# Performance work log

Measured on AMD Instinct MI355X. Metric: run time of the kernel, lower is better.

Reference implementation:

```python
import jax, jax.numpy as jnp
import numpy as np

K = 512
DIM = 256
BETA = 0.25


def setup_inputs() -> dict:
    key = jax.random.key(0)
    k1, k2 = jax.random.split(key)
    x = jax.random.normal(k1, (64, DIM, 32, 32), dtype=jnp.float32)
    lookup_table = jax.random.normal(k2, (K, DIM), dtype=jnp.float32)
    return {"x": x, "lookup_table": lookup_table}


def reference(x, lookup_table):
    b, d, h, w = x.shape
    # [b,d,h,w] -> [b*h*w, d]
    xf = jnp.transpose(x, (0, 2, 3, 1)).reshape(-1, d)
    # Squared Euclidean distances (argmin identical to torch.cdist argmin)
    d2 = (
        jnp.sum(xf * xf, axis=-1, keepdims=True)
        - 2.0 * (xf @ lookup_table.T)
        + jnp.sum(lookup_table * lookup_table, axis=-1)
    )  # [N, K]
    q = jnp.argmin(d2, axis=1)  # [N]
    x_e = lookup_table[q].reshape(b, h, w, d).transpose(0, 3, 1, 2)  # [b,d,h,w]
    q_x = q.reshape(b, h, w)
    codebook_loss = jnp.mean(jnp.square(jax.lax.stop_gradient(x) - x_e))
    commitment_loss = jnp.mean(jnp.square(x - jax.lax.stop_gradient(x_e)))
    loss = codebook_loss + BETA * commitment_loss
    return x_e, q_x, loss
```

## Files before the change

### kernel.cpp

```cpp
#include <hip/hip_runtime.h>

#define DIM     256
#define HW      1024
#define N_ROWS  65536
#define NT      256
#define QBM     64
#define NBLK    1024
#define MARGIN  0.0625f

#define OUT_Q_OFF    16777216
#define OUT_LOSS_OFF 16842752

#define WS_DIST   512
#define WS_X2     1536
#define WS_CNT_I  3072
#define WS_LIST_I 4096
#define WS_LUTBF_B 524288

#define VQ_LDS 73728

typedef __attribute__((ext_vector_type(8))) short short8v;
typedef __attribute__((ext_vector_type(4))) float floatx4;

#define GLOAD_LDS16(gaddr, laddr) \
    __builtin_amdgcn_global_load_lds((const __attribute__((address_space(1))) unsigned int*)(gaddr), \
                                     (__attribute__((address_space(3))) unsigned int*)(laddr), 16, 0, 0)

__device__ __forceinline__ unsigned short bf16_rne(float f) {
    unsigned int u = __float_as_uint(f);
    u += 0x7fffu + ((u >> 16) & 1u);
    return (unsigned short)(u >> 16);
}
__device__ __forceinline__ float bf16_to_f(unsigned short h) {
    return __uint_as_float(((unsigned int)h) << 16);
}
__device__ __forceinline__ uint4 pack8(const unsigned short* h) {
    uint4 u;
    u.x = (unsigned)h[0] | ((unsigned)h[1] << 16);
    u.y = (unsigned)h[2] | ((unsigned)h[3] << 16);
    u.z = (unsigned)h[4] | ((unsigned)h[5] << 16);
    u.w = (unsigned)h[6] | ((unsigned)h[7] << 16);
    return u;
}

__global__ void c2_kernel(const float* __restrict__ lut, float* __restrict__ ws) {
    if (threadIdx.x == 0) ((int*)ws)[WS_CNT_I] = 0;
    int t = threadIdx.x;
    for (int k = t; k < 512; k += 256) {
        const float4* row = (const float4*)(lut + (size_t)k * DIM);
        float s = 0.f;
        #pragma unroll 8
        for (int i = 0; i < DIM / 4; ++i) {
            float4 v = row[i];
            s += v.x * v.x + v.y * v.y + v.z * v.z + v.w * v.w;
        }
        ws[k] = s;
    }
}

__global__ void lutprep_kernel(const float* __restrict__ lut, float* __restrict__ ws) {
    int g = blockIdx.x * 256 + threadIdx.x;
    int lane = g & 63;
    int ctu  = (g >> 6) & 31;
    int dcg  = g >> 11;
    int code = ctu * 16 + (lane & 15);
    int d0   = dcg * 32 + (lane >> 4) * 8;
    const float* src = lut + (size_t)code * DIM + d0;
    unsigned short hi[8], lo[8];
    #pragma unroll
    for (int j = 0; j < 8; ++j) {
        float v = src[j];
        unsigned short h = bf16_rne(v);
        hi[j] = h;
        lo[j] = bf16_rne(v - bf16_to_f(h));
    }
    char* dst = (char*)ws + WS_LUTBF_B + (size_t)((dcg * 32 + ctu) * 2) * 1024 + lane * 16;
    *(uint4*)dst          = pack8(hi);
    *(uint4*)(dst + 1024) = pack8(lo);
}

__global__ __launch_bounds__(NT, 2) void vq_kernel(const float* __restrict__ x,
                                                   const float* __restrict__ lut,
                                                   float* __restrict__ out,
                                                   float* __restrict__ ws) {
    extern __shared__ char smem[];

    const char* lutbf = (const char*)ws + WS_LUTBF_B;

    const int tid = threadIdx.x;
    const int blk = blockIdx.x;
    const int n0  = blk * QBM;
    const int b   = n0 >> 10;
    const int hw0 = n0 & 1023;
    const float* xb = x + (size_t)b * (DIM * HW) + hw0;

    const int wave = tid >> 6;
    const int lane = tid & 63;
    const int l15  = lane & 15;
    const int l4   = lane >> 4;
    const int cg   = wave;

    const int srt  = tid >> 6;
    char* awr_hi = smem + 65536 + srt * 2048 + lane * 16;
    const int arow = srt * 16 + l15;
    const int ad0  = l4 * 8;

    float x2local = 0.f;
    floatx4 acc[4][8];
    #pragma unroll
    for (int i = 0; i < 4; ++i)
        #pragma unroll
        for (int j = 0; j < 8; ++j) acc[i][j] = (floatx4)0.f;

    {
        #pragma unroll
        for (int i = 0; i < 16; ++i) {
            int cc = (tid >> 6) * 16 + i;
            GLOAD_LDS16(lutbf + (size_t)(0 * 64 + cc) * 1024 + lane * 16, smem + cc * 1024);
        }
        const float* src = xb + (size_t)ad0 * HW + arow;
        unsigned short hi[8], lo[8];
        #pragma unroll
        for (int e = 0; e < 8; ++e) {
            float v = src[(size_t)e * HW];
            x2local = fmaf(v, v, x2local);
            unsigned short h = bf16_rne(v);
            hi[e] = h;
            lo[e] = bf16_rne(v - bf16_to_f(h));
        }
        *(uint4*)awr_hi          = pack8(hi);
        *(uint4*)(awr_hi + 1024) = pack8(lo);
    }
    __syncthreads();

    for (int dc = 0; dc < 8; ++dc) {
        short8v ah[4], al[4];
        #pragma unroll
        for (int rtl = 0; rtl < 4; ++rtl) {
            const char* ra = smem + 65536 + rtl * 2048 + lane * 16;
            ah[rtl] = *(const short8v*)ra;
            al[rtl] = *(const short8v*)(ra + 1024);
        }
        short8v bh[8], bl[8];
        #pragma unroll
        for (int ct = 0; ct < 8; ++ct) {
            const char* bp = smem + (size_t)((cg * 8 + ct) * 2) * 1024 + lane * 16;
            bh[ct] = *(const short8v*)bp;
            bl[ct] = *(const short8v*)(bp + 1024);
        }
        __builtin_amdgcn_sched_barrier(0);
        asm volatile("s_waitcnt lgkmcnt(0)" ::: "memory");
        __builtin_amdgcn_sched_barrier(0);
        __builtin_amdgcn_s_barrier();
        __builtin_amdgcn_sched_barrier(0);
        float xn[8];
        if (dc < 7) {
            #pragma unroll
            for (int i = 0; i < 16; ++i) {
                int cc = (tid >> 6) * 16 + i;
                GLOAD_LDS16(lutbf + (size_t)((dc + 1) * 64 + cc) * 1024 + lane * 16, smem + cc * 1024);
            }
            const float* src = xb + (size_t)((dc + 1) * 32 + ad0) * HW + arow;
            #pragma unroll
            for (int e = 0; e < 8; ++e) xn[e] = src[(size_t)e * HW];
        }
        __builtin_amdgcn_s_setprio(1);
        #pragma unroll
        for (int ct = 0; ct < 8; ++ct)
            #pragma unroll
            for (int rtl = 0; rtl < 4; ++rtl)
                acc[rtl][ct] = __builtin_amdgcn_mfma_f32_16x16x32_bf16(ah[rtl], bh[ct], acc[rtl][ct], 0, 0, 0);
        #pragma unroll
        for (int ct = 0; ct < 8; ++ct)
            #pragma unroll
            for (int rtl = 0; rtl < 4; ++rtl)
                acc[rtl][ct] = __builtin_amdgcn_mfma_f32_16x16x32_bf16(al[rtl], bh[ct], acc[rtl][ct], 0, 0, 0);
        #pragma unroll
        for (int ct = 0; ct < 8; ++ct)
            #pragma unroll
            for (int rtl = 0; rtl < 4; ++rtl)
                acc[rtl][ct] = __builtin_amdgcn_mfma_f32_16x16x32_bf16(ah[rtl], bl[ct], acc[rtl][ct], 0, 0, 0);
        __builtin_amdgcn_s_setprio(0);
        if (dc < 7) {
            unsigned short hi[8], lo[8];
            #pragma unroll
            for (int e = 0; e < 8; ++e) {
                float v = xn[e];
                x2local = fmaf(v, v, x2local);
                unsigned short h = bf16_rne(v);
                hi[e] = h;
                lo[e] = bf16_rne(v - bf16_to_f(h));
            }
            *(uint4*)awr_hi          = pack8(hi);
            *(uint4*)(awr_hi + 1024) = pack8(lo);
        }
        __syncthreads();
    }

    float* redv1 = (float*)smem;
    float* redv2 = (float*)(smem + 1024);
    int*   redi1 = (int*)(smem + 2048);
    int*   qsh   = (int*)(smem + 3072);
    float* wsumx = (float*)(smem + 3328);

    #pragma unroll
    for (int rtl = 0; rtl < 4; ++rtl) {
        #pragma unroll
        for (int r = 0; r < 4; ++r) {
            float v1 = 3.4e38f, v2 = 3.4e38f; int i1 = 0;
            #pragma unroll
            for (int ct = 0; ct < 8; ++ct) {
                int code = (cg * 8 + ct) * 16 + l15;
                float dist = fmaf(-2.f, acc[rtl][ct][r], ws[code]);
                if (dist < v1) { v2 = v1; v1 = dist; i1 = code; }
                else if (dist < v2) v2 = dist;
            }
            #pragma unroll
            for (int off = 1; off < 16; off <<= 1) {
                float ov1 = __shfl_xor(v1, off, 64);
                int   oi1 = __shfl_xor(i1, off, 64);
                float ov2 = __shfl_xor(v2, off, 64);
                float nv2 = fminf(fmaxf(v1, ov1), fminf(v2, ov2));
                if (ov1 < v1 || (ov1 == v1 && oi1 < i1)) { v1 = ov1; i1 = oi1; }
                v2 = nv2;
            }
            if (l15 == 0) {
                int idx = cg * 64 + rtl * 16 + l4 * 4 + r;
                redv1[idx] = v1; redi1[idx] = i1; redv2[idx] = v2;
            }
        }
    }
    __syncthreads();

    float dist_part = 0.f;
    if (tid < QBM) {
        const int row = tid;
        float v1 = redv1[row]; int i1 = redi1[row]; float v2 = redv2[row];
        #pragma unroll
        for (int s = 1; s < 4; ++s) {
            float ov1 = redv1[s * 64 + row]; int oi1 = redi1[s * 64 + row]; float ov2 = redv2[s * 64 + row];
            float nv2 = fminf(fmaxf(v1, ov1), fminf(v2, ov2));
            if (ov1 < v1 || (ov1 == v1 && oi1 < i1)) { v1 = ov1; i1 = oi1; }
            v2 = nv2;
        }
        qsh[row] = i1;
        out[OUT_Q_OFF + n0 + row] = (float)i1;
        if (v2 - v1 <= MARGIN) {
            int idx = atomicAdd((int*)ws + WS_CNT_I, 1);
            ((int*)ws)[WS_LIST_I + idx] = n0 + row;
        }
        dist_part = v1;
    }
    float dv = dist_part;
    #pragma unroll
    for (int off = 32; off; off >>= 1) dv += __shfl_down(dv, off, 64);
    if (tid == 0) ws[WS_DIST + blk] = dv;

    float xv = x2local;
    #pragma unroll
    for (int off = 32; off; off >>= 1) xv += __shfl_down(xv, off, 64);
    if (lane == 0) wsumx[wave] = xv;
    __syncthreads();
    if (tid == 0) ws[WS_X2 + blk] = wsumx[0] + wsumx[1] + wsumx[2] + wsumx[3];

    {
        const int row = tid & 63;
        const int dg  = tid >> 6;
        const int q   = qsh[row];
        const float* crow = lut + (size_t)q * DIM;
        float* ob = out + (size_t)b * (DIM * HW) + hw0 + row;
        #pragma unroll 4
        for (int i = 0; i < 16; ++i) {
            int d0 = dg * 64 + i * 4;
            float4 c = *(const float4*)(crow + d0);
            ob[(size_t)(d0 + 0) * HW] = c.x;
            ob[(size_t)(d0 + 1) * HW] = c.y;
            ob[(size_t)(d0 + 2) * HW] = c.z;
            ob[(size_t)(d0 + 3) * HW] = c.w;
        }
    }
}

__global__ void exact_kernel(const float* __restrict__ x, const float* __restrict__ lut,
                             float* __restrict__ out, const float* __restrict__ ws) {
    __shared__ float xr[DIM];
    __shared__ float rv[256];
    __shared__ int   ri[256];
    const int cnt = ((const int*)ws)[WS_CNT_I];
    const int* list = (const int*)ws + WS_LIST_I;
    const int tid = threadIdx.x;
    for (int ii = blockIdx.x; ii < cnt; ii += gridDim.x) {
        const int row = list[ii];
        const int b = row >> 10, hw = row & 1023;
        __syncthreads();
        xr[tid] = x[(size_t)b * (DIM * HW) + (size_t)tid * HW + hw];
        __syncthreads();
        float bv = 3.4e38f; int bi = 0;
        #pragma unroll
        for (int k2 = 0; k2 < 2; ++k2) {
            int k = tid + k2 * 256;
            const float* cr = lut + (size_t)k * DIM;
            float dot = 0.f;
            for (int d = 0; d < DIM; ++d) dot = fmaf(xr[d], cr[d], dot);
            float dist = fmaf(-2.f, dot, ws[k]);
            if (dist < bv || (dist == bv && k < bi)) { bv = dist; bi = k; }
        }
        rv[tid] = bv; ri[tid] = bi;
        __syncthreads();
        for (int s = 128; s; s >>= 1) {
            if (tid < s) {
                float ov = rv[tid + s]; int oi = ri[tid + s];
                if (ov < rv[tid] || (ov == rv[tid] && oi < ri[tid])) {
                    rv[tid] = ov; ri[tid] = oi;
                }
            }
            __syncthreads();
        }
        const int q = ri[0];
        if (tid == 0) out[OUT_Q_OFF + row] = (float)q;
        out[(size_t)b * (DIM * HW) + (size_t)tid * HW + hw] = lut[(size_t)q * DIM + tid];
    }
}

__global__ void loss_kernel(float* __restrict__ out, const float* __restrict__ ws) {
    __shared__ float wsum[4];
    int tid = threadIdx.x;
    float s = 0.f;
    for (int i = tid; i < 2048; i += 256) s += ws[WS_DIST + i];
    #pragma unroll
    for (int off = 32; off; off >>= 1) s += __shfl_down(s, off, 64);
    if ((tid & 63) == 0) wsum[tid >> 6] = s;
    __syncthreads();
    if (tid == 0) {
        float total = wsum[0] + wsum[1] + wsum[2] + wsum[3];
        out[OUT_LOSS_OFF] = total * (1.25f / 16777216.f);
    }
}

extern "C" void kernel_launch(void* const* d_in, const int* in_sizes, int n_in,
                              void* d_out, int out_size, void* d_ws, size_t ws_size,
                              hipStream_t stream) {
    const float* x   = (const float*)d_in[0];
    const float* lut = (const float*)d_in[1];
    float* out = (float*)d_out;
    float* ws  = (float*)d_ws;

    (void)hipFuncSetAttribute((const void*)vq_kernel,
                              hipFuncAttributeMaxDynamicSharedMemorySize, VQ_LDS);

    c2_kernel<<<1, 256, 0, stream>>>(lut, ws);
    lutprep_kernel<<<64, 256, 0, stream>>>(lut, ws);
    vq_kernel<<<NBLK, NT, VQ_LDS, stream>>>(x, lut, out, ws);
    exact_kernel<<<1024, 256, 0, stream>>>(x, lut, out, ws);
    loss_kernel<<<1, 256, 0, stream>>>(out, ws);
}
```

Baseline: 145.2 us.

## Replace split-bf16 3-pass MFMA with single-pass fp16 and smaller row tiles

Switches the distance GEMM from a hi/lo bf16 split that needed three MFMAs per tile to a single fp16 MFMA pass, halving LUT staging bytes. It also halves the row tile to 32 rows per block (2048 blocks), preloads the whole x tile into LDS up front, drops the software-pipelined prefetch in favour of a simple load/sync/compute loop, and raises launch bounds to 3 blocks per CU. The ambiguity margin widens to 0.25 so more rows fall back to the exact fp32 recheck kernel, which adds work there and risks more atomics and list entries.

```diff
diff --git a/kernel.cpp b/kernel.cpp
--- a/kernel.cpp
+++ b/kernel.cpp
@@ -4,44 +4,27 @@
 #define HW      1024
 #define N_ROWS  65536
 #define NT      256
-#define QBM     64
-#define NBLK    1024
-#define MARGIN  0.0625f
+#define QBM     32
+#define NBLK    2048
+#define MARGIN  0.25f
 
 #define OUT_Q_OFF    16777216
 #define OUT_LOSS_OFF 16842752
 
 #define WS_DIST   512
-#define WS_X2     1536
-#define WS_CNT_I  3072
-#define WS_LIST_I 4096
-#define WS_LUTBF_B 524288
-
-#define VQ_LDS 73728
-
-typedef __attribute__((ext_vector_type(8))) short short8v;
-typedef __attribute__((ext_vector_type(4))) float floatx4;
+#define WS_X2     2560
+#define WS_CNT_I  4608
+#define WS_LIST_I 5120
+#define WS_LUTH_B 524288
+
+#define VQ_LDS 49152
+
+typedef _Float16 half8v __attribute__((ext_vector_type(8)));
+typedef float floatx4 __attribute__((ext_vector_type(4)));
 
 #define GLOAD_LDS16(gaddr, laddr) \
     __builtin_amdgcn_global_load_lds((const __attribute__((address_space(1))) unsigned int*)(gaddr), \
                                      (__attribute__((address_space(3))) unsigned int*)(laddr), 16, 0, 0)
-
-__device__ __forceinline__ unsigned short bf16_rne(float f) {
-    unsigned int u = __float_as_uint(f);
-    u += 0x7fffu + ((u >> 16) & 1u);
-    return (unsigned short)(u >> 16);
-}
-__device__ __forceinline__ float bf16_to_f(unsigned short h) {
-    return __uint_as_float(((unsigned int)h) << 16);
-}
-__device__ __forceinline__ uint4 pack8(const unsigned short* h) {
-    uint4 u;
-    u.x = (unsigned)h[0] | ((unsigned)h[1] << 16);
-    u.y = (unsigned)h[2] | ((unsigned)h[3] << 16);
-    u.z = (unsigned)h[4] | ((unsigned)h[5] << 16);
-    u.w = (unsigned)h[6] | ((unsigned)h[7] << 16);
-    return u;
-}
 
 __global__ void c2_kernel(const float* __restrict__ lut, float* __restrict__ ws) {
     if (threadIdx.x == 0) ((int*)ws)[WS_CNT_I] = 0;
@@ -66,26 +49,21 @@
     int code = ctu * 16 + (lane & 15);
     int d0   = dcg * 32 + (lane >> 4) * 8;
     const float* src = lut + (size_t)code * DIM + d0;
-    unsigned short hi[8], lo[8];
-    #pragma unroll
-    for (int j = 0; j < 8; ++j) {
-        float v = src[j];
-        unsigned short h = bf16_rne(v);
-        hi[j] = h;
-        lo[j] = bf16_rne(v - bf16_to_f(h));
-    }
-    char* dst = (char*)ws + WS_LUTBF_B + (size_t)((dcg * 32 + ctu) * 2) * 1024 + lane * 16;
-    *(uint4*)dst          = pack8(hi);
-    *(uint4*)(dst + 1024) = pack8(lo);
-}
-
-__global__ __launch_bounds__(NT, 2) void vq_kernel(const float* __restrict__ x,
+    half8v h;
+    #pragma unroll
+    for (int j = 0; j < 8; ++j) h[j] = (_Float16)src[j];
+    char* dst = (char*)ws + WS_LUTH_B + (size_t)(dcg * 32 + ctu) * 1024 + lane * 16;
+    *(half8v*)dst = h;
+}
+
+__global__ __launch_bounds__(NT, 3) void vq_kernel(const float* __restrict__ x,
                                                    const float* __restrict__ lut,
                                                    float* __restrict__ out,
                                                    float* __restrict__ ws) {
     extern __shared__ char smem[];
 
-    const char* lutbf = (const char*)ws + WS_LUTBF_B;
+    const char* luth = (const char*)ws + WS_LUTH_B;
+    char* asm_ = smem + 32768;
 
     const int tid = threadIdx.x;
     const int blk = blockIdx.x;
@@ -100,111 +78,62 @@
     const int l4   = lane >> 4;
     const int cg   = wave;
 
-    const int srt  = tid >> 6;
-    char* awr_hi = smem + 65536 + srt * 2048 + lane * 16;
-    const int arow = srt * 16 + l15;
-    const int ad0  = l4 * 8;
-
     float x2local = 0.f;
-    floatx4 acc[4][8];
-    #pragma unroll
-    for (int i = 0; i < 4; ++i)
+    {
+        const int srow = tid & 31;
+        const int sdg  = tid >> 5;
+        const float* src = xb + (size_t)(sdg * 32) * HW + srow;
+        char* abase = asm_ + (size_t)((srow >> 4) * 8 + sdg) * 1024 + (srow & 15) * 16;
+        #pragma unroll
+        for (int eg = 0; eg < 4; ++eg) {
+            half8v h;
+            #pragma unroll
+            for (int j = 0; j < 8; ++j) {
+                float v = src[(size_t)(eg * 8 + j) * HW];
+                x2local = fmaf(v, v, x2local);
+                h[j] = (_Float16)v;
+            }
+            *(half8v*)(abase + eg * 256) = h;
+        }
+    }
+
+    floatx4 acc[2][8];
+    #pragma unroll
+    for (int i = 0; i < 2; ++i)
         #pragma unroll
         for (int j = 0; j < 8; ++j) acc[i][j] = (floatx4)0.f;
 
-    {
-        #pragma unroll
-        for (int i = 0; i < 16; ++i) {
-            int cc = (tid >> 6) * 16 + i;
-            GLOAD_LDS16(lutbf + (size_t)(0 * 64 + cc) * 1024 + lane * 16, smem + cc * 1024);
-        }
-        const float* src = xb + (size_t)ad0 * HW + arow;
-        unsigned short hi[8], lo[8];
-        #pragma unroll
-        for (int e = 0; e < 8; ++e) {
-            float v = src[(size_t)e * HW];
-            x2local = fmaf(v, v, x2local);
-            unsigned short h = bf16_rne(v);
-            hi[e] = h;
-            lo[e] = bf16_rne(v - bf16_to_f(h));
-        }
-        *(uint4*)awr_hi          = pack8(hi);
-        *(uint4*)(awr_hi + 1024) = pack8(lo);
-    }
-    __syncthreads();
-
     for (int dc = 0; dc < 8; ++dc) {
-        short8v ah[4], al[4];
-        #pragma unroll
-        for (int rtl = 0; rtl < 4; ++rtl) {
-            const char* ra = smem + 65536 + rtl * 2048 + lane * 16;
-            ah[rtl] = *(const short8v*)ra;
-            al[rtl] = *(const short8v*)(ra + 1024);
-        }
-        short8v bh[8], bl[8];
-        #pragma unroll
-        for (int ct = 0; ct < 8; ++ct) {
-            const char* bp = smem + (size_t)((cg * 8 + ct) * 2) * 1024 + lane * 16;
-            bh[ct] = *(const short8v*)bp;
-            bl[ct] = *(const short8v*)(bp + 1024);
-        }
-        __builtin_amdgcn_sched_barrier(0);
-        asm volatile("s_waitcnt lgkmcnt(0)" ::: "memory");
-        __builtin_amdgcn_sched_barrier(0);
-        __builtin_amdgcn_s_barrier();
-        __builtin_amdgcn_sched_barrier(0);
-        float xn[8];
-        if (dc < 7) {
-            #pragma unroll
-            for (int i = 0; i < 16; ++i) {
-                int cc = (tid >> 6) * 16 + i;
-                GLOAD_LDS16(lutbf + (size_t)((dc + 1) * 64 + cc) * 1024 + lane * 16, smem + cc * 1024);
-            }
-            const float* src = xb + (size_t)((dc + 1) * 32 + ad0) * HW + arow;
-            #pragma unroll
-            for (int e = 0; e < 8; ++e) xn[e] = src[(size_t)e * HW];
-        }
-        __builtin_amdgcn_s_setprio(1);
+        __syncthreads();
+        #pragma unroll
+        for (int i = 0; i < 8; ++i) {
+            int cc = wave * 8 + i;
+            GLOAD_LDS16(luth + (size_t)(dc * 32 + cc) * 1024 + lane * 16, smem + cc * 1024);
+        }
+        __syncthreads();
+        half8v ah[2], bh[8];
+        #pragma unroll
+        for (int rtl = 0; rtl < 2; ++rtl)
+            ah[rtl] = *(const half8v*)(asm_ + (size_t)(rtl * 8 + dc) * 1024 + lane * 16);
         #pragma unroll
         for (int ct = 0; ct < 8; ++ct)
-            #pragma unroll
-            for (int rtl = 0; rtl < 4; ++rtl)
-                acc[rtl][ct] = __builtin_amdgcn_mfma_f32_16x16x32_bf16(ah[rtl], bh[ct], acc[rtl][ct], 0, 0, 0);
+            bh[ct] = *(const half8v*)(smem + (size_t)(cg * 8 + ct) * 1024 + lane * 16);
         #pragma unroll
         for (int ct = 0; ct < 8; ++ct)
             #pragma unroll
-            for (int rtl = 0; rtl < 4; ++rtl)
-                acc[rtl][ct] = __builtin_amdgcn_mfma_f32_16x16x32_bf16(al[rtl], bh[ct], acc[rtl][ct], 0, 0, 0);
-        #pragma unroll
-        for (int ct = 0; ct < 8; ++ct)
-            #pragma unroll
-            for (int rtl = 0; rtl < 4; ++rtl)
-                acc[rtl][ct] = __builtin_amdgcn_mfma_f32_16x16x32_bf16(ah[rtl], bl[ct], acc[rtl][ct], 0, 0, 0);
-        __builtin_amdgcn_s_setprio(0);
-        if (dc < 7) {
-            unsigned short hi[8], lo[8];
-            #pragma unroll
-            for (int e = 0; e < 8; ++e) {
-                float v = xn[e];
-                x2local = fmaf(v, v, x2local);
-                unsigned short h = bf16_rne(v);
-                hi[e] = h;
-                lo[e] = bf16_rne(v - bf16_to_f(h));
-            }
-            *(uint4*)awr_hi          = pack8(hi);
-            *(uint4*)(awr_hi + 1024) = pack8(lo);
-        }
-        __syncthreads();
-    }
+            for (int rtl = 0; rtl < 2; ++rtl)
+                acc[rtl][ct] = __builtin_amdgcn_mfma_f32_16x16x32_f16(ah[rtl], bh[ct], acc[rtl][ct], 0, 0, 0);
+    }
+    __syncthreads();
 
     float* redv1 = (float*)smem;
-    float* redv2 = (float*)(smem + 1024);
-    int*   redi1 = (int*)(smem + 2048);
-    int*   qsh   = (int*)(smem + 3072);
-    float* wsumx = (float*)(smem + 3328);
-
-    #pragma unroll
-    for (int rtl = 0; rtl < 4; ++rtl) {
+    float* redv2 = (float*)(smem + 512);
+    int*   redi1 = (int*)(smem + 1024);
+    int*   qsh   = (int*)(smem + 1536);
+    float* wsumx = (float*)(smem + 1664);
+
+    #pragma unroll
+    for (int rtl = 0; rtl < 2; ++rtl) {
         #pragma unroll
         for (int r = 0; r < 4; ++r) {
             float v1 = 3.4e38f, v2 = 3.4e38f; int i1 = 0;
@@ -225,7 +154,7 @@
                 v2 = nv2;
             }
             if (l15 == 0) {
-                int idx = cg * 64 + rtl * 16 + l4 * 4 + r;
+                int idx = cg * 32 + rtl * 16 + l4 * 4 + r;
                 redv1[idx] = v1; redi1[idx] = i1; redv2[idx] = v2;
             }
         }
@@ -238,7 +167,7 @@
         float v1 = redv1[row]; int i1 = redi1[row]; float v2 = redv2[row];
         #pragma unroll
         for (int s = 1; s < 4; ++s) {
-            float ov1 = redv1[s * 64 + row]; int oi1 = redi1[s * 64 + row]; float ov2 = redv2[s * 64 + row];
+            float ov1 = redv1[s * 32 + row]; int oi1 = redi1[s * 32 + row]; float ov2 = redv2[s * 32 + row];
             float nv2 = fminf(fmaxf(v1, ov1), fminf(v2, ov2));
             if (ov1 < v1 || (ov1 == v1 && oi1 < i1)) { v1 = ov1; i1 = oi1; }
             v2 = nv2;
@@ -264,14 +193,14 @@
     if (tid == 0) ws[WS_X2 + blk] = wsumx[0] + wsumx[1] + wsumx[2] + wsumx[3];
 
     {
-        const int row = tid & 63;
-        const int dg  = tid >> 6;
+        const int row = tid & 31;
+        const int dg  = tid >> 5;
         const int q   = qsh[row];
         const float* crow = lut + (size_t)q * DIM;
         float* ob = out + (size_t)b * (DIM * HW) + hw0 + row;
         #pragma unroll 4
-        for (int i = 0; i < 16; ++i) {
-            int d0 = dg * 64 + i * 4;
+        for (int i = 0; i < 8; ++i) {
+            int d0 = dg * 32 + i * 4;
             float4 c = *(const float4*)(crow + d0);
             ob[(size_t)(d0 + 0) * HW] = c.x;
             ob[(size_t)(d0 + 1) * HW] = c.y;
@@ -326,7 +255,7 @@
     __shared__ float wsum[4];
     int tid = threadIdx.x;
     float s = 0.f;
-    for (int i = tid; i < 2048; i += 256) s += ws[WS_DIST + i];
+    for (int i = tid; i < 4096; i += 256) s += ws[WS_DIST + i];
     #pragma unroll
     for (int off = 32; off; off >>= 1) s += __shfl_down(s, off, 64);
     if ((tid & 63) == 0) wsum[tid >> 6] = s;
@@ -351,6 +280,6 @@
     c2_kernel<<<1, 256, 0, stream>>>(lut, ws);
     lutprep_kernel<<<64, 256, 0, stream>>>(lut, ws);
     vq_kernel<<<NBLK, NT, VQ_LDS, stream>>>(x, lut, out, ws);
-    exact_kernel<<<1024, 256, 0, stream>>>(x, lut, out, ws);
+    exact_kernel<<<2048, 256, 0, stream>>>(x, lut, out, ws);
     loss_kernel<<<1, 256, 0, stream>>>(out, ws);
 }
```

Result: slower. 192.1 us (+32.4%).
